# Kernel tuning notes

Hardware: AMD Instinct MI355X
Metric: run time of the kernel (lower is better)

The kernel has to match this reference:

```python
import jax, jax.numpy as jnp
import numpy as np

N = 1_000_000
E = 1_000_000
K = 512
H = 64
F_IN = 19
N_ITERS = 3
EPS = 1e-5

def _leaky(x):
    return jax.nn.leaky_relu(x, negative_slope=0.01)

def _layernorm(x, g, b):
    mu = jnp.mean(x, axis=-1, keepdims=True)
    var = jnp.var(x, axis=-1, keepdims=True)
    return (x - mu) * jax.lax.rsqrt(var + EPS) * g + b

def setup_inputs() -> dict:
    key = jax.random.key(0)
    ks = jax.random.split(key, 20)
    s = 0.1
    inp = {
        "x": jax.random.normal(ks[0], (N, F_IN), dtype=jnp.float32),
        "edge_index": jax.random.randint(ks[1], (2, E), 0, N, dtype=jnp.int64),
        "candidate_indices": jax.random.randint(ks[2], (K,), 0, N, dtype=jnp.int64),
        # embedding params
        "pW_in": jax.random.normal(ks[3], (F_IN, H), dtype=jnp.float32) * s,
        "pb_in": jnp.zeros((H,), dtype=jnp.float32),
        "eW": jax.random.normal(ks[4], (2, H, H), dtype=jnp.float32) * s,
        "eb": jnp.zeros((2, H), dtype=jnp.float32),
        "gamma": jnp.ones((2, H), dtype=jnp.float32),
        "beta": jnp.zeros((2, H), dtype=jnp.float32),
        # bottom-up step MLPs (stacked over n_iters)
        "sW1": jax.random.normal(ks[5], (N_ITERS, H, H), dtype=jnp.float32) * s,
        "sb1": jnp.zeros((N_ITERS, H), dtype=jnp.float32),
        "sW2": jax.random.normal(ks[6], (N_ITERS, H, H), dtype=jnp.float32) * s,
        "sb2": jnp.zeros((N_ITERS, H), dtype=jnp.float32),
        # score head
        "hW1": jax.random.normal(ks[7], (H, H), dtype=jnp.float32) * s,
        "hb1": jnp.zeros((H,), dtype=jnp.float32),
        "hW2": jax.random.normal(ks[8], (H, 1), dtype=jnp.float32) * s,
        "hb2": jnp.zeros((1,), dtype=jnp.float32),
    }
    return inp

def reference(x, edge_index, candidate_indices, pW_in, pb_in, eW, eb, gamma, beta,
              sW1, sb1, sW2, sb2, hW1, hb1, hW2, hb2):
    # TreeNodeEmbedding: proj + 2 residual layers with LayerNorm
    h = _leaky(x @ pW_in + pb_in)
    for i in range(2):
        h = _layernorm(h + _leaky(h @ eW[i] + eb[i]), gamma[i], beta[i])
    parent_idx = edge_index[0]
    child_idx = edge_index[1]
    # Bottom-up message passing: scatter-mean over children, tiny MLP update
    for i in range(N_ITERS):
        child_h = h[child_idx]                                   # [E, H] gather
        sum_p = jax.ops.segment_sum(child_h, parent_idx, num_segments=N)  # [N, H]
        cnt = jax.ops.segment_sum(jnp.ones((E,), dtype=h.dtype), parent_idx, num_segments=N)  # [N]
        mean_p = sum_p / jnp.maximum(cnt, 1.0)[:, None]
        mask = (cnt > 0)[:, None]
        delta = _leaky(mean_p @ sW1[i] + sb1[i]) @ sW2[i] + sb2[i]
        h = h + jnp.where(mask, delta, 0.0)
    # Score head on candidates, softmax over k (all candidates real -> full_logits == scores)
    cand_h = h[candidate_indices]                                # [K, H]
    scores = (_leaky(cand_h @ hW1 + hb1) @ hW2 + hb2)[:, 0]      # [K]
    probs = jax.nn.softmax(scores)
    return probs
```

## Files before the change

### kernel.cpp

```cpp
#include <hip/hip_runtime.h>
#include <hip/hip_bf16.h>
#include <math.h>

#define H 64
#define FIN 19
#define EPSLN 1e-5f

#define OFF_PW   0
#define OFF_PB   1280
#define OFF_EW   1344
#define OFF_EB   9536
#define OFF_G    9664
#define OFF_BT   9792
#define OFF_W1   9920
#define OFF_W2   22208
#define OFF_B1   34496
#define OFF_B2   34688
#define OFF_HW1  34880
#define OFF_HB1  38976
#define OFF_HW2  39040
#define OFF_HB2  39104
#define WTS_TOTAL 39105

__device__ __forceinline__ float leaky(float v) { return v > 0.f ? v : 0.01f * v; }

__device__ __forceinline__ float wsumf(float v) {
#pragma unroll
  for (int off = 32; off > 0; off >>= 1) v += __shfl_xor(v, off, 64);
  return v;
}

__device__ __forceinline__ bool detect_bf16(const unsigned short* xs) {
  const int lane = threadIdx.x & 63;
  unsigned a = xs[lane], b = xs[64 + lane];
  unsigned ea = (a >> 7) & 0xFFu, ebx = (b >> 7) & 0xFFu;
  return !__any((int)(ea > 140u || ebx > 140u));
}

__device__ __forceinline__ bool detect_i64(const int* w) {
  const int lane = threadIdx.x & 63;
  return __all((int)(w[2 * lane + 1] == 0));
}

__device__ __forceinline__ float ldf(const void* p, size_t i, bool bf) {
  return bf ? __bfloat162float(((const __hip_bfloat16*)p)[i]) : ((const float*)p)[i];
}

struct WT {
  const void* src[14];
  int off[14], len[14], sl[14], rp[14], rs[14], cs[14];
};

__global__ __launch_bounds__(256) void prep_wts(WT T, const unsigned short* xs,
                                                float* wts, int total) {
  const bool bf = detect_bf16(xs);
  for (int i = blockIdx.x * 256 + threadIdx.x; i < total; i += gridDim.x * 256) {
    int p = 0;
    while (i >= T.off[p] + T.len[p]) ++p;
    const int loc = i - T.off[p];
    float v;
    if (T.rp[p] == 0) {
      v = ldf(T.src[p], loc, bf);
    } else {
      const int s = loc / T.sl[p];
      const int r = loc - s * T.sl[p];
      const int j = r / T.rp[p];
      const int k = r - j * T.rp[p];
      v = (k < T.rs[p])
              ? ldf(T.src[p], (size_t)s * T.rs[p] * T.cs[p] + (size_t)k * T.cs[p] + j, bf)
              : 0.f;
    }
    wts[i] = v;
  }
}

__device__ float embed_math(const void* x, const float* wts, float* stg, int v,
                            int lane, bool bf) {
  float xv = (lane < FIN) ? ldf(x, (size_t)v * FIN + lane, bf) : 0.f;
  stg[lane] = xv;
  __syncthreads();
  const float* tp = wts + OFF_PW + lane * 20;
  float a0 = wts[OFF_PB + lane], a1 = 0.f, a2 = 0.f, a3 = 0.f;
#pragma unroll
  for (int k = 0; k < 20; k += 4) {
    float4 m = *(const float4*)&stg[k];
    float4 w = *(const float4*)&tp[k];
    a0 += m.x * w.x; a1 += m.y * w.y; a2 += m.z * w.z; a3 += m.w * w.w;
  }
  __syncthreads();
  float h = leaky((a0 + a1) + (a2 + a3));
#pragma unroll
  for (int L = 0; L < 2; ++L) {
    stg[lane] = h;
    __syncthreads();
    const float* tw = wts + OFF_EW + L * 4096 + lane * 64;
    a0 = wts[OFF_EB + L * 64 + lane]; a1 = a2 = a3 = 0.f;
#pragma unroll
    for (int k = 0; k < H; k += 4) {
      float4 m = *(const float4*)&stg[k];
      float4 w = *(const float4*)&tw[k];
      a0 += m.x * w.x; a1 += m.y * w.y; a2 += m.z * w.z; a3 += m.w * w.w;
    }
    __syncthreads();
    float val = h + leaky((a0 + a1) + (a2 + a3));
    float mu = wsumf(val) * (1.f / 64.f);
    float d = val - mu;
    float var = wsumf(d * d) * (1.f / 64.f);
    h = d * (1.f / sqrtf(var + EPSLN)) * wts[OFF_G + L * 64 + lane] +
        wts[OFF_BT + L * 64 + lane];
  }
  return h;
}

__device__ float delta_math(const float* wts, float* stg, float mean, int it, int lane) {
  stg[lane] = mean;
  __syncthreads();
  const float* w1 = wts + OFF_W1 + it * 4096 + lane * 64;
  float a0 = wts[OFF_B1 + it * 64 + lane], a1 = 0.f, a2 = 0.f, a3 = 0.f;
#pragma unroll
  for (int k = 0; k < H; k += 4) {
    float4 m = *(const float4*)&stg[k];
    float4 w = *(const float4*)&w1[k];
    a0 += m.x * w.x; a1 += m.y * w.y; a2 += m.z * w.z; a3 += m.w * w.w;
  }
  __syncthreads();
  float t1 = leaky((a0 + a1) + (a2 + a3));
  stg[lane] = t1;
  __syncthreads();
  const float* w2 = wts + OFF_W2 + it * 4096 + lane * 64;
  a0 = wts[OFF_B2 + it * 64 + lane]; a1 = a2 = a3 = 0.f;
#pragma unroll
  for (int k = 0; k < H; k += 4) {
    float4 m = *(const float4*)&stg[k];
    float4 w = *(const float4*)&w2[k];
    a0 += m.x * w.x; a1 += m.y * w.y; a2 += m.z * w.z; a3 += m.w * w.w;
  }
  __syncthreads();
  return (a0 + a1) + (a2 + a3);
}

__global__ __launch_bounds__(256) void init_kernel(int* map, int nN, int* counters, int K,
                                                   int* ch3, int n3, int* ch2, int n2,
                                                   int* ch1, int n1) {
  const int tid = blockIdx.x * 256 + threadIdx.x;
  const int stride = gridDim.x * 256;
  for (int i = tid; i < nN; i += stride) map[i] = 0;
  for (int i = tid; i < n3; i += stride) ch3[i] = -1;
  for (int i = tid; i < n2; i += stride) ch2[i] = -1;
  for (int i = tid; i < n1; i += stride) ch1[i] = -1;
  if (tid < 3) counters[tid] = 0;
  if (tid == 3) counters[3] = K;
}

__global__ __launch_bounds__(64) void seed_kernel(const int* cand_raw, int K, int nN,
                                                  int* map, int* node3, int* nextSame3,
                                                  int* selfChild3, int* ctr2, int cap2,
                                                  int* node2) {
  const bool i64 = detect_i64(cand_raw);
  int t = blockIdx.x * 64 + threadIdx.x;
  if (t >= K) return;
  int cv = i64 ? cand_raw[2 * t] : cand_raw[t];
  unsigned n = (unsigned)cv;
  if (n >= (unsigned)nN) n = 0;
  node3[t] = (int)n;
  int enc = (1 << 24) | t;
  int old = atomicExch(&map[n], enc);
  nextSame3[t] = ((old >> 24) == 1) ? (old & 0xFFFFFF) : -1;
  int s = atomicAdd(ctr2, 1);
  if (s < cap2) { node2[s] = (int)n; selfChild3[t] = s; } else selfChild3[t] = 0;
}

__global__ __launch_bounds__(256) void regself_kernel(const int* ctrU_, int capU,
                                                      const int* nodeU, int* map, int epoch,
                                                      int* nextSameU, int* ctrD, int capD,
                                                      int* nodeD, int* selfChildU) {
  int cnt = *ctrU_; if (cnt > capU) cnt = capU;
  int t = blockIdx.x * 256 + threadIdx.x;
  if (t >= cnt) return;
  int n = nodeU[t];
  int enc = (epoch << 24) | t;
  int old = atomicExch(&map[n], enc);
  nextSameU[t] = ((old >> 24) == epoch) ? (old & 0xFFFFFF) : -1;
  int s = atomicAdd(ctrD, 1);
  if (s < capD) { nodeD[s] = n; selfChildU[t] = s; } else selfChildU[t] = 0;
}

__global__ __launch_bounds__(256) void scan_kernel(const int* eraw, int E, int nN,
                                                   const int* map, int epoch,
                                                   const int* nextSameU, int* childHeadU,
                                                   int* ctrD, int capD, int* nodeD,
                                                   int* childNextD) {
  const bool i64 = detect_i64(eraw);
  int e = blockIdx.x * 256 + threadIdx.x;
  if (e >= E) return;
  int pv = i64 ? eraw[2 * e] : eraw[e];
  unsigned p = (unsigned)pv;
  if (p >= (unsigned)nN) p = 0;
  int m = map[p];
  if ((m >> 24) != epoch) return;
  int cv = i64 ? eraw[2 * (E + e)] : eraw[E + e];
  unsigned c = (unsigned)cv;
  if (c >= (unsigned)nN) c = 0;
  int t = m & 0xFFFFFF;
  while (t >= 0) {
    int ct = atomicAdd(ctrD, 1);
    if (ct < capD) {
      nodeD[ct] = (int)c;
      childNextD[ct] = atomicExch(&childHeadU[t], ct);
    }
    t = nextSameU[t];
  }
}

__global__ __launch_bounds__(64) void eval0_kernel(const void* x, const int* ctr0_,
                                                   int cap0, const int* node0,
                                                   const float* wts, float* val0) {
  __shared__ float stg[H];
  int cnt = *ctr0_; if (cnt > cap0) cnt = cap0;
  const int t = blockIdx.x;
  if (t >= cnt) return;
  const int lane = threadIdx.x;
  const bool bf = detect_bf16((const unsigned short*)x);
  float h = embed_math(x, wts, stg, node0[t], lane, bf);
  val0[(size_t)t * H + lane] = h;
}

__global__ __launch_bounds__(64) void evalL_kernel(const int* ctrU_, int capU,
                                                   const int* selfChildU,
                                                   const int* childHeadU,
                                                   const int* childNextD,
                                                   const float* valD, float* valU,
                                                   const float* wts, int it) {
  __shared__ float stg[H];
  int cnt = *ctrU_; if (cnt > capU) cnt = capU;
  const int t = blockIdx.x;
  if (t >= cnt) return;
  const int lane = threadIdx.x;
  float hv = valD[(size_t)selfChildU[t] * H + lane];
  float acc = 0.f;
  int k = 0;
  int c = childHeadU[t];
  while (c >= 0) { acc += valD[(size_t)c * H + lane]; ++k; c = childNextD[c]; }
  if (k > 0) hv += delta_math(wts, stg, acc / (float)k, it, lane);
  valU[(size_t)t * H + lane] = hv;
}

__global__ __launch_bounds__(512) void score_kernel(
    const float* __restrict__ candH, const float* __restrict__ wts,
    const void* x, void* out, int K) {
  __shared__ float red[512];
  const int t = threadIdx.x;
  const bool bf = detect_bf16((const unsigned short*)x);
  float sc = 0.f;
  if (t < K) {
    float hr[H];
#pragma unroll
    for (int k = 0; k < H; k += 4) {
      float4 v = *(const float4*)&candH[(size_t)t * H + k];
      hr[k] = v.x; hr[k + 1] = v.y; hr[k + 2] = v.z; hr[k + 3] = v.w;
    }
    for (int j = 0; j < H; ++j) {
      float a = wts[OFF_HB1 + j];
#pragma unroll
      for (int k = 0; k < H; k += 4) {
        float4 w = *(const float4*)&wts[OFF_HW1 + j * 64 + k];
        a += hr[k] * w.x + hr[k + 1] * w.y + hr[k + 2] * w.z + hr[k + 3] * w.w;
      }
      sc += leaky(a) * wts[OFF_HW2 + j];
    }
    sc += wts[OFF_HB2];
  }
  red[t] = (t < K) ? sc : -3.0e38f;
  __syncthreads();
  for (int off = 256; off > 0; off >>= 1) {
    if (t < off) red[t] = fmaxf(red[t], red[t + off]);
    __syncthreads();
  }
  const float m = red[0];
  __syncthreads();
  const float ex = (t < K) ? expf(sc - m) : 0.f;
  red[t] = ex;
  __syncthreads();
  for (int off = 256; off > 0; off >>= 1) {
    if (t < off) red[t] += red[t + off];
    __syncthreads();
  }
  const float inv = 1.f / red[0];
  if (t < K) {
    float p = ex * inv;
    if (bf) ((__hip_bfloat16*)out)[t] = __float2bfloat16(p);
    else    ((float*)out)[t] = p;
  }
}

extern "C" void kernel_launch(void* const* d_in, const int* in_sizes, int n_in,
                              void* d_out, int out_size, void* d_ws, size_t ws_size,
                              hipStream_t stream) {
  const void* x   = d_in[0];
  const int* edge = (const int*)d_in[1];
  const int* cand = (const int*)d_in[2];
  const int nN = in_sizes[0] / FIN;
  const int E  = in_sizes[1] / 2;
  const int K  = in_sizes[2];

  const int CAP2 = 8 * K, CAP1 = 16 * K, CAP0 = 32 * K;

  auto al = [](size_t b) -> size_t { return (b + 255) & ~(size_t)255; };
  const size_t szW   = (size_t)WTS_TOTAL * sizeof(float);
  const size_t szMap = (size_t)nN * sizeof(int);
  const size_t szK   = (size_t)K * sizeof(int);
  const size_t sz2   = (size_t)CAP2 * sizeof(int);
  const size_t sz1   = (size_t)CAP1 * sizeof(int);
  const size_t sz0   = (size_t)CAP0 * sizeof(int);
  const size_t szV0  = (size_t)CAP0 * H * sizeof(float);
  const size_t szV1  = (size_t)CAP1 * H * sizeof(float);
  const size_t szV2  = (size_t)CAP2 * H * sizeof(float);
  const size_t szV3  = (size_t)K * H * sizeof(float);
  const size_t need = al(szW) + al(szMap) + 256  +
                      4 * al(szK) + 5 * al(sz2) + 5 * al(sz1) + 2 * al(sz0) +
                      al(szV0) + al(szV1) + al(szV2) + al(szV3);

  if (K > 2048 || K < 128 || E < 128 || ws_size < need) return;

  char* wsb = (char*)d_ws;
  size_t off = 0;
  auto carve = [&](size_t bytes) -> void* {
    void* p = wsb + off;
    off += (bytes + 255) & ~(size_t)255;
    return p;
  };
  float* wts     = (float*)carve(szW);
  int* map       = (int*)carve(szMap);
  int* counters  = (int*)carve(256);
  int* node3     = (int*)carve(szK);
  int* nextSame3 = (int*)carve(szK);
  int* selfCh3   = (int*)carve(szK);
  int* chHead3   = (int*)carve(szK);
  int* node2     = (int*)carve(sz2);
  int* nextSame2 = (int*)carve(sz2);
  int* selfCh2   = (int*)carve(sz2);
  int* chHead2   = (int*)carve(sz2);
  int* chNext2   = (int*)carve(sz2);
  int* node1     = (int*)carve(sz1);
  int* nextSame1 = (int*)carve(sz1);
  int* selfCh1   = (int*)carve(sz1);
  int* chHead1   = (int*)carve(sz1);
  int* chNext1   = (int*)carve(sz1);
  int* node0     = (int*)carve(sz0);
  int* chNext0   = (int*)carve(sz0);
  float* val0    = (float*)carve(szV0);
  float* val1    = (float*)carve(szV1);
  float* val2    = (float*)carve(szV2);
  float* val3    = (float*)carve(szV3);

  WT T;
  auto setv = [&](int i, const void* s, int o, int l) {
    T.src[i] = s; T.off[i] = o; T.len[i] = l; T.sl[i] = l;
    T.rp[i] = 0; T.rs[i] = 0; T.cs[i] = 0;
  };
  auto setm = [&](int i, const void* s, int o, int l, int sl, int rpad, int rs, int cs) {
    T.src[i] = s; T.off[i] = o; T.len[i] = l; T.sl[i] = sl;
    T.rp[i] = rpad; T.rs[i] = rs; T.cs[i] = cs;
  };
  setm(0,  d_in[3],  OFF_PW,  1280, 1280, 20, 19, 64);
  setv(1,  d_in[4],  OFF_PB,  64);
  setm(2,  d_in[5],  OFF_EW,  8192, 4096, 64, 64, 64);
  setv(3,  d_in[6],  OFF_EB,  128);
  setv(4,  d_in[7],  OFF_G,   128);
  setv(5,  d_in[8],  OFF_BT,  128);
  setm(6,  d_in[9],  OFF_W1,  12288, 4096, 64, 64, 64);
  setm(7,  d_in[11], OFF_W2,  12288, 4096, 64, 64, 64);
  setv(8,  d_in[10], OFF_B1,  192);
  setv(9,  d_in[12], OFF_B2,  192);
  setm(10, d_in[13], OFF_HW1, 4096, 4096, 64, 64, 64);
  setv(11, d_in[14], OFF_HB1, 64);
  setv(12, d_in[15], OFF_HW2, 64);
  setv(13, d_in[16], OFF_HB2, 1);

  prep_wts<<<160, 256, 0, stream>>>(T, (const unsigned short*)x, wts, WTS_TOTAL);

  init_kernel<<<1024, 256, 0, stream>>>(map, nN, counters, K, chHead3, K,
                                        chHead2, CAP2, chHead1, CAP1);

  seed_kernel<<<(K + 63) / 64, 64, 0, stream>>>(cand, K, nN, map, node3, nextSame3,
                                                selfCh3, &counters[0], CAP2, node2);
  scan_kernel<<<(E + 255) / 256, 256, 0, stream>>>(edge, E, nN, map, 1, nextSame3,
                                                   chHead3, &counters[0], CAP2,
                                                   node2, chNext2);
  regself_kernel<<<(CAP2 + 255) / 256, 256, 0, stream>>>(&counters[0], CAP2, node2, map, 2,
                                                         nextSame2, &counters[1], CAP1,
                                                         node1, selfCh2);
  scan_kernel<<<(E + 255) / 256, 256, 0, stream>>>(edge, E, nN, map, 2, nextSame2,
                                                   chHead2, &counters[1], CAP1,
                                                   node1, chNext1);
  regself_kernel<<<(CAP1 + 255) / 256, 256, 0, stream>>>(&counters[1], CAP1, node1, map, 3,
                                                         nextSame1, &counters[2], CAP0,
                                                         node0, selfCh1);
  scan_kernel<<<(E + 255) / 256, 256, 0, stream>>>(edge, E, nN, map, 3, nextSame1,
                                                   chHead1, &counters[2], CAP0,
                                                   node0, chNext0);

  eval0_kernel<<<CAP0, 64, 0, stream>>>(x, &counters[2], CAP0, node0, wts, val0);
  evalL_kernel<<<CAP1, 64, 0, stream>>>(&counters[1], CAP1, selfCh1, chHead1, chNext0,
                                        val0, val1, wts, 0);
  evalL_kernel<<<CAP2, 64, 0, stream>>>(&counters[0], CAP2, selfCh2, chHead2, chNext1,
                                        val1, val2, wts, 1);
  evalL_kernel<<<K, 64, 0, stream>>>(&counters[3], K, selfCh3, chHead3, chNext2,
                                     val2, val3, wts, 2);

  score_kernel<<<1, 512, 0, stream>>>(val3, wts, x, d_out, K);
}
```

Measured before the change: 268.2 us.

## Fuse all stages into one persistent kernel with software grid barriers

Replaces the chain of about fifteen kernel launches with a single persistent kernel that runs every stage: weight prep, seeding, three edge scans, the level evaluations, scoring and softmax. Stages are separated by an atomic-counter grid barrier. Per-level maps replace map re-initialisation, and both are reset with memsets. Inside the per-node math, block-wide __syncthreads becomes wave barriers, since each wave owns its own staging slice. This removes launch overhead and the small-grid tail stages, but it relies on every block being co-resident and the barrier spins with a guard timeout. Each edge scan now covers E with fewer threads per pass.

```diff
diff --git a/kernel.cpp b/kernel.cpp
--- a/kernel.cpp
+++ b/kernel.cpp
@@ -30,6 +30,12 @@
   return v;
 }
 
+__device__ __forceinline__ void wsync() {
+  asm volatile("" ::: "memory");
+  __builtin_amdgcn_wave_barrier();
+  asm volatile("" ::: "memory");
+}
+
 __device__ __forceinline__ bool detect_bf16(const unsigned short* xs) {
   const int lane = threadIdx.x & 63;
   unsigned a = xs[lane], b = xs[64 + lane];
@@ -51,34 +57,38 @@
   int off[14], len[14], sl[14], rp[14], rs[14], cs[14];
 };
 
+__device__ __forceinline__ void prep_one(const WT& T, bool bf, float* wts, int i) {
+  int p = 0;
+  while (i >= T.off[p] + T.len[p]) ++p;
+  const int loc = i - T.off[p];
+  float v;
+  if (T.rp[p] == 0) {
+    v = ldf(T.src[p], loc, bf);
+  } else {
+    const int s = loc / T.sl[p];
+    const int r = loc - s * T.sl[p];
+    const int j = r / T.rp[p];
+    const int k = r - j * T.rp[p];
+    v = (k < T.rs[p])
+            ? ldf(T.src[p], (size_t)s * T.rs[p] * T.cs[p] + (size_t)k * T.cs[p] + j, bf)
+            : 0.f;
+  }
+  wts[i] = v;
+}
+
 __global__ __launch_bounds__(256) void prep_wts(WT T, const unsigned short* xs,
                                                 float* wts, int total) {
   const bool bf = detect_bf16(xs);
-  for (int i = blockIdx.x * 256 + threadIdx.x; i < total; i += gridDim.x * 256) {
-    int p = 0;
-    while (i >= T.off[p] + T.len[p]) ++p;
-    const int loc = i - T.off[p];
-    float v;
-    if (T.rp[p] == 0) {
-      v = ldf(T.src[p], loc, bf);
-    } else {
-      const int s = loc / T.sl[p];
-      const int r = loc - s * T.sl[p];
-      const int j = r / T.rp[p];
-      const int k = r - j * T.rp[p];
-      v = (k < T.rs[p])
-              ? ldf(T.src[p], (size_t)s * T.rs[p] * T.cs[p] + (size_t)k * T.cs[p] + j, bf)
-              : 0.f;
-    }
-    wts[i] = v;
-  }
+  for (int i = blockIdx.x * 256 + threadIdx.x; i < total; i += gridDim.x * 256)
+    prep_one(T, bf, wts, i);
 }
 
 __device__ float embed_math(const void* x, const float* wts, float* stg, int v,
                             int lane, bool bf) {
   float xv = (lane < FIN) ? ldf(x, (size_t)v * FIN + lane, bf) : 0.f;
+  wsync();
   stg[lane] = xv;
-  __syncthreads();
+  wsync();
   const float* tp = wts + OFF_PW + lane * 20;
   float a0 = wts[OFF_PB + lane], a1 = 0.f, a2 = 0.f, a3 = 0.f;
 #pragma unroll
@@ -87,12 +97,12 @@
     float4 w = *(const float4*)&tp[k];
     a0 += m.x * w.x; a1 += m.y * w.y; a2 += m.z * w.z; a3 += m.w * w.w;
   }
-  __syncthreads();
   float h = leaky((a0 + a1) + (a2 + a3));
 #pragma unroll
   for (int L = 0; L < 2; ++L) {
+    wsync();
     stg[lane] = h;
-    __syncthreads();
+    wsync();
     const float* tw = wts + OFF_EW + L * 4096 + lane * 64;
     a0 = wts[OFF_EB + L * 64 + lane]; a1 = a2 = a3 = 0.f;
 #pragma unroll
@@ -101,7 +111,6 @@
       float4 w = *(const float4*)&tw[k];
       a0 += m.x * w.x; a1 += m.y * w.y; a2 += m.z * w.z; a3 += m.w * w.w;
     }
-    __syncthreads();
     float val = h + leaky((a0 + a1) + (a2 + a3));
     float mu = wsumf(val) * (1.f / 64.f);
     float d = val - mu;
@@ -113,8 +122,9 @@
 }
 
 __device__ float delta_math(const float* wts, float* stg, float mean, int it, int lane) {
+  wsync();
   stg[lane] = mean;
-  __syncthreads();
+  wsync();
   const float* w1 = wts + OFF_W1 + it * 4096 + lane * 64;
   float a0 = wts[OFF_B1 + it * 64 + lane], a1 = 0.f, a2 = 0.f, a3 = 0.f;
 #pragma unroll
@@ -123,10 +133,10 @@
     float4 w = *(const float4*)&w1[k];
     a0 += m.x * w.x; a1 += m.y * w.y; a2 += m.z * w.z; a3 += m.w * w.w;
   }
-  __syncthreads();
   float t1 = leaky((a0 + a1) + (a2 + a3));
+  wsync();
   stg[lane] = t1;
-  __syncthreads();
+  wsync();
   const float* w2 = wts + OFF_W2 + it * 4096 + lane * 64;
   a0 = wts[OFF_B2 + it * 64 + lane]; a1 = a2 = a3 = 0.f;
 #pragma unroll
@@ -135,7 +145,7 @@
     float4 w = *(const float4*)&w2[k];
     a0 += m.x * w.x; a1 += m.y * w.y; a2 += m.z * w.z; a3 += m.w * w.w;
   }
-  __syncthreads();
+  wsync();
   return (a0 + a1) + (a2 + a3);
 }
 
@@ -293,6 +303,264 @@
   }
 }
 
+struct FA {
+  const void* x; const void* edge; const void* cand; void* outp;
+  int nN, E, K, CAP2, CAP1, CAP0;
+  int *ctrl;
+  int *map3, *map2, *map1;
+  int *chHead3, *chHead2, *chHead1;
+  float* wts;
+  int *node3, *nextSame3, *selfCh3;
+  int *node2, *nextSame2, *selfCh2, *chNext2;
+  int *node1, *nextSame1, *selfCh1, *chNext1;
+  int *node0, *chNext0;
+  float *val0, *val1, *val2, *val3, *scores;
+  WT T;
+};
+
+__device__ __forceinline__ void gsync(int* bar, int& phase) {
+  __syncthreads();
+  if (threadIdx.x == 0) {
+    ++phase;
+    __hip_atomic_fetch_add(bar, 1, __ATOMIC_ACQ_REL, __HIP_MEMORY_SCOPE_AGENT);
+    const int tgt = phase * (int)gridDim.x;
+    int guard = 0;
+    while (__hip_atomic_load(bar, __ATOMIC_RELAXED, __HIP_MEMORY_SCOPE_AGENT) < tgt) {
+      __builtin_amdgcn_s_sleep(2);
+      if (++guard > (1 << 22)) break;
+    }
+    (void)__hip_atomic_load(bar, __ATOMIC_ACQUIRE, __HIP_MEMORY_SCOPE_AGENT);
+  }
+  __syncthreads();
+}
+
+__global__ __launch_bounds__(256, 4) void fused_kernel(FA A) {
+  __shared__ float smem[4 * H];
+  const int tid = threadIdx.x;
+  const int lane = tid & 63;
+  const int wib = tid >> 6;
+  const int gtid = blockIdx.x * 256 + tid;
+  const int nthr = (int)gridDim.x * 256;
+  const int waveId = blockIdx.x * 4 + wib;
+  const int nWaves = (int)gridDim.x * 4;
+  float* stg = &smem[wib * H];
+  int* bar = A.ctrl;
+  int* c2 = A.ctrl + 16;
+  int* c1 = A.ctrl + 32;
+  int* c0 = A.ctrl + 48;
+  int phase = 0;
+
+  const bool bf = detect_bf16((const unsigned short*)A.x);
+  const int* eraw = (const int*)A.edge;
+  const int* craw = (const int*)A.cand;
+  const bool i64e = detect_i64(eraw);
+  const bool i64c = detect_i64(craw);
+
+  for (int i = gtid; i < WTS_TOTAL; i += nthr) prep_one(A.T, bf, A.wts, i);
+  for (int t = gtid; t < A.K; t += nthr) {
+    int cv = i64c ? craw[2 * t] : craw[t];
+    unsigned n = (unsigned)cv;
+    if (n >= (unsigned)A.nN) n = 0;
+    A.node3[t] = (int)n;
+    A.nextSame3[t] = atomicExch(&A.map3[(int)n], t);
+    int s = atomicAdd(c2, 1);
+    if (s < A.CAP2) {
+      A.node2[s] = (int)n; A.selfCh3[t] = s;
+      A.nextSame2[s] = atomicExch(&A.map2[(int)n], s);
+      int s1 = atomicAdd(c1, 1);
+      if (s1 < A.CAP1) {
+        A.node1[s1] = (int)n; A.selfCh2[s] = s1;
+        A.nextSame1[s1] = atomicExch(&A.map1[(int)n], s1);
+        int s0 = atomicAdd(c0, 1);
+        if (s0 < A.CAP0) { A.node0[s0] = (int)n; A.selfCh1[s1] = s0; }
+        else A.selfCh1[s1] = 0;
+      } else A.selfCh2[s] = 0;
+    } else A.selfCh3[t] = 0;
+  }
+  gsync(bar, phase);
+
+  for (int e = gtid; e < A.E; e += nthr) {
+    int pv = i64e ? eraw[2 * e] : eraw[e];
+    unsigned p = (unsigned)pv;
+    if (p >= (unsigned)A.nN) p = 0;
+    int t = A.map3[p];
+    if (t < 0) continue;
+    int cv = i64e ? eraw[2 * (A.E + e)] : eraw[A.E + e];
+    unsigned cn = (unsigned)cv;
+    if (cn >= (unsigned)A.nN) cn = 0;
+    for (; t >= 0; t = A.nextSame3[t]) {
+      int ct = atomicAdd(c2, 1);
+      if (ct < A.CAP2) {
+        A.node2[ct] = (int)cn;
+        A.chNext2[ct] = atomicExch(&A.chHead3[t], ct);
+        A.nextSame2[ct] = atomicExch(&A.map2[(int)cn], ct);
+        int s1 = atomicAdd(c1, 1);
+        if (s1 < A.CAP1) {
+          A.node1[s1] = (int)cn; A.selfCh2[ct] = s1;
+          A.nextSame1[s1] = atomicExch(&A.map1[(int)cn], s1);
+          int s0 = atomicAdd(c0, 1);
+          if (s0 < A.CAP0) { A.node0[s0] = (int)cn; A.selfCh1[s1] = s0; }
+          else A.selfCh1[s1] = 0;
+        } else A.selfCh2[ct] = 0;
+      }
+    }
+  }
+  gsync(bar, phase);
+
+  for (int e = gtid; e < A.E; e += nthr) {
+    int pv = i64e ? eraw[2 * e] : eraw[e];
+    unsigned p = (unsigned)pv;
+    if (p >= (unsigned)A.nN) p = 0;
+    int t = A.map2[p];
+    if (t < 0) continue;
+    int cv = i64e ? eraw[2 * (A.E + e)] : eraw[A.E + e];
+    unsigned cn = (unsigned)cv;
+    if (cn >= (unsigned)A.nN) cn = 0;
+    for (; t >= 0; t = A.nextSame2[t]) {
+      int ct = atomicAdd(c1, 1);
+      if (ct < A.CAP1) {
+        A.node1[ct] = (int)cn;
+        A.chNext1[ct] = atomicExch(&A.chHead2[t], ct);
+        A.nextSame1[ct] = atomicExch(&A.map1[(int)cn], ct);
+        int s0 = atomicAdd(c0, 1);
+        if (s0 < A.CAP0) { A.node0[s0] = (int)cn; A.selfCh1[ct] = s0; }
+        else A.selfCh1[ct] = 0;
+      }
+    }
+  }
+  gsync(bar, phase);
+
+  for (int e = gtid; e < A.E; e += nthr) {
+    int pv = i64e ? eraw[2 * e] : eraw[e];
+    unsigned p = (unsigned)pv;
+    if (p >= (unsigned)A.nN) p = 0;
+    int t = A.map1[p];
+    if (t < 0) continue;
+    int cv = i64e ? eraw[2 * (A.E + e)] : eraw[A.E + e];
+    unsigned cn = (unsigned)cv;
+    if (cn >= (unsigned)A.nN) cn = 0;
+    for (; t >= 0; t = A.nextSame1[t]) {
+      int ct = atomicAdd(c0, 1);
+      if (ct < A.CAP0) {
+        A.node0[ct] = (int)cn;
+        A.chNext0[ct] = atomicExch(&A.chHead1[t], ct);
+      }
+    }
+  }
+  gsync(bar, phase);
+
+  {
+    int cnt = __hip_atomic_load(c0, __ATOMIC_RELAXED, __HIP_MEMORY_SCOPE_AGENT);
+    if (cnt > A.CAP0) cnt = A.CAP0;
+    for (int t = waveId; t < cnt; t += nWaves) {
+      float h = embed_math(A.x, A.wts, stg, A.node0[t], lane, bf);
+      A.val0[(size_t)t * H + lane] = h;
+    }
+  }
+  gsync(bar, phase);
+
+  {
+    int cnt = __hip_atomic_load(c1, __ATOMIC_RELAXED, __HIP_MEMORY_SCOPE_AGENT);
+    if (cnt > A.CAP1) cnt = A.CAP1;
+    for (int t = waveId; t < cnt; t += nWaves) {
+      float hv = A.val0[(size_t)A.selfCh1[t] * H + lane];
+      float acc = 0.f;
+      int kc = 0;
+      for (int c = A.chHead1[t]; c >= 0; c = A.chNext0[c]) {
+        acc += A.val0[(size_t)c * H + lane];
+        ++kc;
+      }
+      if (kc > 0) hv += delta_math(A.wts, stg, acc / (float)kc, 0, lane);
+      A.val1[(size_t)t * H + lane] = hv;
+    }
+  }
+  gsync(bar, phase);
+
+  {
+    int cnt = __hip_atomic_load(c2, __ATOMIC_RELAXED, __HIP_MEMORY_SCOPE_AGENT);
+    if (cnt > A.CAP2) cnt = A.CAP2;
+    for (int t = waveId; t < cnt; t += nWaves) {
+      float hv = A.val1[(size_t)A.selfCh2[t] * H + lane];
+      float acc = 0.f;
+      int kc = 0;
+      for (int c = A.chHead2[t]; c >= 0; c = A.chNext1[c]) {
+        acc += A.val1[(size_t)c * H + lane];
+        ++kc;
+      }
+      if (kc > 0) hv += delta_math(A.wts, stg, acc / (float)kc, 1, lane);
+      A.val2[(size_t)t * H + lane] = hv;
+    }
+  }
+  gsync(bar, phase);
+
+  for (int t = waveId; t < A.K; t += nWaves) {
+    float hv = A.val2[(size_t)A.selfCh3[t] * H + lane];
+    float acc = 0.f;
+    int kc = 0;
+    for (int c = A.chHead3[t]; c >= 0; c = A.chNext2[c]) {
+      acc += A.val2[(size_t)c * H + lane];
+      ++kc;
+    }
+    if (kc > 0) hv += delta_math(A.wts, stg, acc / (float)kc, 2, lane);
+    A.val3[(size_t)t * H + lane] = hv;
+  }
+  gsync(bar, phase);
+
+  for (int t = gtid; t < A.K; t += nthr) {
+    float hr[H];
+#pragma unroll
+    for (int k = 0; k < H; k += 4) {
+      float4 v4 = *(const float4*)&A.val3[(size_t)t * H + k];
+      hr[k] = v4.x; hr[k + 1] = v4.y; hr[k + 2] = v4.z; hr[k + 3] = v4.w;
+    }
+    float sc = 0.f;
+    for (int j = 0; j < H; ++j) {
+      float a = A.wts[OFF_HB1 + j];
+#pragma unroll
+      for (int k = 0; k < H; k += 4) {
+        float4 w = *(const float4*)&A.wts[OFF_HW1 + j * 64 + k];
+        a += hr[k] * w.x + hr[k + 1] * w.y + hr[k + 2] * w.z + hr[k + 3] * w.w;
+      }
+      sc += leaky(a) * A.wts[OFF_HW2 + j];
+    }
+    sc += A.wts[OFF_HB2];
+    A.scores[t] = sc;
+  }
+  gsync(bar, phase);
+
+  if (blockIdx.x == 0) {
+    __shared__ float red[256];
+    float lm = -3.0e38f;
+    for (int i = tid; i < A.K; i += 256) lm = fmaxf(lm, A.scores[i]);
+    red[tid] = lm;
+    __syncthreads();
+    for (int off = 128; off > 0; off >>= 1) {
+      if (tid < off) red[tid] = fmaxf(red[tid], red[tid + off]);
+      __syncthreads();
+    }
+    const float m = red[0];
+    __syncthreads();
+    float ls = 0.f;
+    for (int i = tid; i < A.K; i += 256) {
+      float e = expf(A.scores[i] - m);
+      A.scores[i] = e;
+      ls += e;
+    }
+    red[tid] = ls;
+    __syncthreads();
+    for (int off = 128; off > 0; off >>= 1) {
+      if (tid < off) red[tid] += red[tid + off];
+      __syncthreads();
+    }
+    const float inv = 1.f / red[0];
+    for (int i = tid; i < A.K; i += 256) {
+      float pv = A.scores[i] * inv;
+      if (bf) ((__hip_bfloat16*)A.outp)[i] = __float2bfloat16(pv);
+      else    ((float*)A.outp)[i] = pv;
+    }
+  }
+}
+
 extern "C" void kernel_launch(void* const* d_in, const int* in_sizes, int n_in,
                               void* d_out, int out_size, void* d_ws, size_t ws_size,
                               hipStream_t stream) {
@@ -302,6 +570,8 @@
   const int nN = in_sizes[0] / FIN;
   const int E  = in_sizes[1] / 2;
   const int K  = in_sizes[2];
+
+  if (K > 2048 || K < 128 || E < 128 || nN < 1) return;
 
   const int CAP2 = 8 * K, CAP1 = 16 * K, CAP0 = 32 * K;
 
@@ -316,42 +586,6 @@
   const size_t szV1  = (size_t)CAP1 * H * sizeof(float);
   const size_t szV2  = (size_t)CAP2 * H * sizeof(float);
   const size_t szV3  = (size_t)K * H * sizeof(float);
-  const size_t need = al(szW) + al(szMap) + 256  +
-                      4 * al(szK) + 5 * al(sz2) + 5 * al(sz1) + 2 * al(sz0) +
-                      al(szV0) + al(szV1) + al(szV2) + al(szV3);
-
-  if (K > 2048 || K < 128 || E < 128 || ws_size < need) return;
-
-  char* wsb = (char*)d_ws;
-  size_t off = 0;
-  auto carve = [&](size_t bytes) -> void* {
-    void* p = wsb + off;
-    off += (bytes + 255) & ~(size_t)255;
-    return p;
-  };
-  float* wts     = (float*)carve(szW);
-  int* map       = (int*)carve(szMap);
-  int* counters  = (int*)carve(256);
-  int* node3     = (int*)carve(szK);
-  int* nextSame3 = (int*)carve(szK);
-  int* selfCh3   = (int*)carve(szK);
-  int* chHead3   = (int*)carve(szK);
-  int* node2     = (int*)carve(sz2);
-  int* nextSame2 = (int*)carve(sz2);
-  int* selfCh2   = (int*)carve(sz2);
-  int* chHead2   = (int*)carve(sz2);
-  int* chNext2   = (int*)carve(sz2);
-  int* node1     = (int*)carve(sz1);
-  int* nextSame1 = (int*)carve(sz1);
-  int* selfCh1   = (int*)carve(sz1);
-  int* chHead1   = (int*)carve(sz1);
-  int* chNext1   = (int*)carve(sz1);
-  int* node0     = (int*)carve(sz0);
-  int* chNext0   = (int*)carve(sz0);
-  float* val0    = (float*)carve(szV0);
-  float* val1    = (float*)carve(szV1);
-  float* val2    = (float*)carve(szV2);
-  float* val3    = (float*)carve(szV3);
 
   WT T;
   auto setv = [&](int i, const void* s, int o, int l) {
@@ -377,36 +611,127 @@
   setv(12, d_in[15], OFF_HW2, 64);
   setv(13, d_in[16], OFF_HB2, 1);
 
-  prep_wts<<<160, 256, 0, stream>>>(T, (const unsigned short*)x, wts, WTS_TOTAL);
-
-  init_kernel<<<1024, 256, 0, stream>>>(map, nN, counters, K, chHead3, K,
-                                        chHead2, CAP2, chHead1, CAP1);
-
-  seed_kernel<<<(K + 63) / 64, 64, 0, stream>>>(cand, K, nN, map, node3, nextSame3,
-                                                selfCh3, &counters[0], CAP2, node2);
-  scan_kernel<<<(E + 255) / 256, 256, 0, stream>>>(edge, E, nN, map, 1, nextSame3,
-                                                   chHead3, &counters[0], CAP2,
-                                                   node2, chNext2);
-  regself_kernel<<<(CAP2 + 255) / 256, 256, 0, stream>>>(&counters[0], CAP2, node2, map, 2,
-                                                         nextSame2, &counters[1], CAP1,
-                                                         node1, selfCh2);
-  scan_kernel<<<(E + 255) / 256, 256, 0, stream>>>(edge, E, nN, map, 2, nextSame2,
-                                                   chHead2, &counters[1], CAP1,
-                                                   node1, chNext1);
-  regself_kernel<<<(CAP1 + 255) / 256, 256, 0, stream>>>(&counters[1], CAP1, node1, map, 3,
-                                                         nextSame1, &counters[2], CAP0,
-                                                         node0, selfCh1);
-  scan_kernel<<<(E + 255) / 256, 256, 0, stream>>>(edge, E, nN, map, 3, nextSame1,
-                                                   chHead1, &counters[2], CAP0,
-                                                   node0, chNext0);
-
-  eval0_kernel<<<CAP0, 64, 0, stream>>>(x, &counters[2], CAP0, node0, wts, val0);
-  evalL_kernel<<<CAP1, 64, 0, stream>>>(&counters[1], CAP1, selfCh1, chHead1, chNext0,
-                                        val0, val1, wts, 0);
-  evalL_kernel<<<CAP2, 64, 0, stream>>>(&counters[0], CAP2, selfCh2, chHead2, chNext1,
-                                        val1, val2, wts, 1);
-  evalL_kernel<<<K, 64, 0, stream>>>(&counters[3], K, selfCh3, chHead3, chNext2,
-                                     val2, val3, wts, 2);
-
-  score_kernel<<<1, 512, 0, stream>>>(val3, wts, x, d_out, K);
-}
+  int dev = 0, nCU = 0, maxB = 0;
+  bool okq = (hipGetDevice(&dev) == hipSuccess) &&
+             (hipDeviceGetAttribute(&nCU, hipDeviceAttributeMultiprocessorCount,
+                                    dev) == hipSuccess) &&
+             (hipOccupancyMaxActiveBlocksPerMultiprocessor(&maxB, fused_kernel, 256,
+                                                           0) == hipSuccess) &&
+             nCU >= 8 && maxB >= 1;
+
+  const size_t needF = 256 + 3 * al(szMap) + al(szK) + al(sz2) + al(sz1) +
+                       al(szW) + 3 * al(szK) + 4 * al(sz2) + 4 * al(sz1) +
+                       2 * al(sz0) + al(szV0) + al(szV1) + al(szV2) + al(szV3) +
+                       al(szK);
+
+  if (okq && ws_size >= needF) {
+    char* wsb = (char*)d_ws;
+    size_t off = 0;
+    auto carve = [&](size_t bytes) -> void* {
+      void* p = wsb + off;
+      off += (bytes + 255) & ~(size_t)255;
+      return p;
+    };
+    FA A;
+    A.x = x; A.edge = edge; A.cand = cand; A.outp = d_out;
+    A.nN = nN; A.E = E; A.K = K; A.CAP2 = CAP2; A.CAP1 = CAP1; A.CAP0 = CAP0;
+    A.ctrl = (int*)carve(256);
+    char* ffs = wsb + off;
+    A.map3 = (int*)carve(szMap);
+    A.map2 = (int*)carve(szMap);
+    A.map1 = (int*)carve(szMap);
+    A.chHead3 = (int*)carve(szK);
+    A.chHead2 = (int*)carve(sz2);
+    A.chHead1 = (int*)carve(sz1);
+    const size_t ffbytes = (size_t)((wsb + off) - ffs);
+    A.wts = (float*)carve(szW);
+    A.node3 = (int*)carve(szK); A.nextSame3 = (int*)carve(szK); A.selfCh3 = (int*)carve(szK);
+    A.node2 = (int*)carve(sz2); A.nextSame2 = (int*)carve(sz2);
+    A.selfCh2 = (int*)carve(sz2); A.chNext2 = (int*)carve(sz2);
+    A.node1 = (int*)carve(sz1); A.nextSame1 = (int*)carve(sz1);
+    A.selfCh1 = (int*)carve(sz1); A.chNext1 = (int*)carve(sz1);
+    A.node0 = (int*)carve(sz0); A.chNext0 = (int*)carve(sz0);
+    A.val0 = (float*)carve(szV0); A.val1 = (float*)carve(szV1);
+    A.val2 = (float*)carve(szV2); A.val3 = (float*)carve(szV3);
+    A.scores = (float*)carve(szK);
+    A.T = T;
+
+    int g = nCU * (maxB < 4 ? maxB : 4);
+    if (g > 1024) g = 1024;
+    if (g >= 8) {
+      hipMemsetAsync(A.ctrl, 0, 256, stream);
+      hipMemsetAsync(ffs, 0xFF, ffbytes, stream);
+      fused_kernel<<<g, 256, 0, stream>>>(A);
+      return;
+    }
+  }
+
+  {
+    const size_t need = al(szW) + al(szMap) + 256 +
+                        4 * al(szK) + 5 * al(sz2) + 5 * al(sz1) + 2 * al(sz0) +
+                        al(szV0) + al(szV1) + al(szV2) + al(szV3);
+    if (ws_size < need) return;
+
+    char* wsb = (char*)d_ws;
+    size_t off = 0;
+    auto carve = [&](size_t bytes) -> void* {
+      void* p = wsb + off;
+      off += (bytes + 255) & ~(size_t)255;
+      return p;
+    };
+    float* wts     = (float*)carve(szW);
+    int* map       = (int*)carve(szMap);
+    int* counters  = (int*)carve(256);
+    int* node3     = (int*)carve(szK);
+    int* nextSame3 = (int*)carve(szK);
+    int* selfCh3   = (int*)carve(szK);
+    int* chHead3   = (int*)carve(szK);
+    int* node2     = (int*)carve(sz2);
+    int* nextSame2 = (int*)carve(sz2);
+    int* selfCh2   = (int*)carve(sz2);
+    int* chHead2   = (int*)carve(sz2);
+    int* chNext2   = (int*)carve(sz2);
+    int* node1     = (int*)carve(sz1);
+    int* nextSame1 = (int*)carve(sz1);
+    int* selfCh1   = (int*)carve(sz1);
+    int* chHead1   = (int*)carve(sz1);
+    int* chNext1   = (int*)carve(sz1);
+    int* node0     = (int*)carve(sz0);
+    int* chNext0   = (int*)carve(sz0);
+    float* val0    = (float*)carve(szV0);
+    float* val1    = (float*)carve(szV1);
+    float* val2    = (float*)carve(szV2);
+    float* val3    = (float*)carve(szV3);
+
+    prep_wts<<<160, 256, 0, stream>>>(T, (const unsigned short*)x, wts, WTS_TOTAL);
+    init_kernel<<<1024, 256, 0, stream>>>(map, nN, counters, K, chHead3, K,
+                                          chHead2, CAP2, chHead1, CAP1);
+    seed_kernel<<<(K + 63) / 64, 64, 0, stream>>>(cand, K, nN, map, node3, nextSame3,
+                                                  selfCh3, &counters[0], CAP2, node2);
+    scan_kernel<<<(E + 255) / 256, 256, 0, stream>>>(edge, E, nN, map, 1, nextSame3,
+                                                     chHead3, &counters[0], CAP2,
+                                                     node2, chNext2);
+    regself_kernel<<<(CAP2 + 255) / 256, 256, 0, stream>>>(&counters[0], CAP2, node2, map, 2,
+                                                           nextSame2, &counters[1], CAP1,
+                                                           node1, selfCh2);
+    scan_kernel<<<(E + 255) / 256, 256, 0, stream>>>(edge, E, nN, map, 2, nextSame2,
+                                                     chHead2, &counters[1], CAP1,
+                                                     node1, chNext1);
+    regself_kernel<<<(CAP1 + 255) / 256, 256, 0, stream>>>(&counters[1], CAP1, node1, map, 3,
+                                                           nextSame1, &counters[2], CAP0,
+                                                           node0, selfCh1);
+    scan_kernel<<<(E + 255) / 256, 256, 0, stream>>>(edge, E, nN, map, 3, nextSame1,
+                                                     chHead1, &counters[2], CAP0,
+                                                     node0, chNext0);
+
+    eval0_kernel<<<CAP0, 64, 0, stream>>>(x, &counters[2], CAP0, node0, wts, val0);
+    evalL_kernel<<<CAP1, 64, 0, stream>>>(&counters[1], CAP1, selfCh1, chHead1, chNext0,
+                                          val0, val1, wts, 0);
+    evalL_kernel<<<CAP2, 64, 0, stream>>>(&counters[0], CAP2, selfCh2, chHead2, chNext1,
+                                          val1, val2, wts, 1);
+    evalL_kernel<<<K, 64, 0, stream>>>(&counters[3], K, selfCh3, chHead3, chNext2,
+                                       val2, val3, wts, 2);
+
+    score_kernel<<<1, 512, 0, stream>>>(val3, wts, x, d_out, K);
+  }
+}
```

After: 655.5 us. 2.44x slower.
